# Kernel optimization log

Measured on AMD Instinct MI355X. Metric: run time of the kernel, lower is better.

Reference implementation:

```python
import jax, jax.numpy as jnp
import numpy as np
import math

NUM_LANDMARKS = 64
HEAD_DIM = 64
NUM_HEAD = 16
BATCH = 4
SEQ_LEN = 4096


def iterative_inv(mat, n_iter=6):
    # mat: [..., m, m]
    I = jnp.eye(mat.shape[-1], dtype=mat.dtype)
    K = mat
    # scalar normalization: global max of column sums * global max of row sums
    scale = 1.0 / (jnp.max(jnp.sum(jnp.abs(K), axis=-2)) * jnp.max(jnp.sum(jnp.abs(K), axis=-1)))
    V = scale * jnp.swapaxes(K, -1, -2)
    for _ in range(n_iter):
        KV = jnp.matmul(K, V)
        V = jnp.matmul(0.25 * V, 13.0 * I - jnp.matmul(KV, 15.0 * I - jnp.matmul(KV, 7.0 * I - KV)))
    return V


def setup_inputs() -> dict:
    key = jax.random.key(0)
    k1, k2, k3 = jax.random.split(key, 3)
    shape = (BATCH, NUM_HEAD, SEQ_LEN, HEAD_DIM)
    Q = jax.random.normal(k1, shape, dtype=jnp.float32)
    K = jax.random.normal(k2, shape, dtype=jnp.float32)
    V = jax.random.normal(k3, shape, dtype=jnp.float32)
    return {"Q": Q, "K": K, "V": V}


def reference(Q, K, V):
    seq_len = Q.shape[-2]
    m = NUM_LANDMARKS
    scale = 1.0 / math.sqrt(math.sqrt(HEAD_DIM))
    Q = Q * scale
    K = K * scale
    # landmark pooling: mean over contiguous segments of length seq_len // m
    seg = seq_len // m
    Q_lm = Q.reshape(-1, NUM_HEAD, m, seg, HEAD_DIM).mean(axis=-2)  # [B,H,m,d]
    K_lm = K.reshape(-1, NUM_HEAD, m, seg, HEAD_DIM).mean(axis=-2)  # [B,H,m,d]
    # three softmax kernels
    kernel_1 = jax.nn.softmax(jnp.einsum('bhsd,bhmd->bhsm', Q, K_lm), axis=-1)   # [B,H,S,m]
    kernel_2 = jax.nn.softmax(jnp.einsum('bhmd,bhnd->bhmn', Q_lm, K_lm), axis=-1)  # [B,H,m,m]
    kernel_3 = jax.nn.softmax(jnp.einsum('bhmd,bhsd->bhms', Q_lm, K), axis=-1)   # [B,H,m,S]
    inv_k2 = iterative_inv(kernel_2)
    X = jnp.matmul(jnp.matmul(kernel_1, inv_k2), jnp.matmul(kernel_3, V))  # [B,H,S,d]
    return X
```

## Files before the change

kernel.cpp:

```cpp
#include <hip/hip_runtime.h>
#include <hip/hip_bf16.h>

#define PAD 68
#define KP  72
#define SCALE 0.35355339059327379f

typedef __attribute__((ext_vector_type(8))) short bf16x8;
typedef __attribute__((ext_vector_type(4))) float f32x4;
#define MFMA_BF16 __builtin_amdgcn_mfma_f32_16x16x32_bf16

__device__ __forceinline__ short f2b(float f) {
    unsigned u = __float_as_uint(f);
    u += 0x7fff + ((u >> 16) & 1);
    return (short)(u >> 16);
}
__device__ __forceinline__ float b2f(short h) {
    return __uint_as_float(((unsigned)(unsigned short)h) << 16);
}

__device__ __forceinline__ void fma16(float acc[16], float a, const float* b) {
    const float4* b4 = reinterpret_cast<const float4*>(b);
    float4 x0 = b4[0], x1 = b4[1], x2 = b4[2], x3 = b4[3];
    acc[0]  += a * x0.x; acc[1]  += a * x0.y; acc[2]  += a * x0.z; acc[3]  += a * x0.w;
    acc[4]  += a * x1.x; acc[5]  += a * x1.y; acc[6]  += a * x1.z; acc[7]  += a * x1.w;
    acc[8]  += a * x2.x; acc[9]  += a * x2.y; acc[10] += a * x2.z; acc[11] += a * x2.w;
    acc[12] += a * x3.x; acc[13] += a * x3.y; acc[14] += a * x3.z; acc[15] += a * x3.w;
}

__device__ __forceinline__ void mm_tile(float acc[4][4],
                                        const float* __restrict__ A, int lda,
                                        const float* __restrict__ B,
                                        int i0, int j0) {
#pragma unroll
    for (int r = 0; r < 4; r++)
#pragma unroll
        for (int c = 0; c < 4; c++) acc[r][c] = 0.f;
#pragma unroll 4
    for (int k0 = 0; k0 < 64; k0 += 4) {
        float4 b0 = *reinterpret_cast<const float4*>(&B[(k0 + 0) * PAD + j0]);
        float4 b1 = *reinterpret_cast<const float4*>(&B[(k0 + 1) * PAD + j0]);
        float4 b2 = *reinterpret_cast<const float4*>(&B[(k0 + 2) * PAD + j0]);
        float4 b3 = *reinterpret_cast<const float4*>(&B[(k0 + 3) * PAD + j0]);
        float4 a0 = *reinterpret_cast<const float4*>(&A[(i0 + 0) * lda + k0]);
        float4 a1 = *reinterpret_cast<const float4*>(&A[(i0 + 1) * lda + k0]);
        float4 a2 = *reinterpret_cast<const float4*>(&A[(i0 + 2) * lda + k0]);
        float4 a3 = *reinterpret_cast<const float4*>(&A[(i0 + 3) * lda + k0]);
#define ROW_UPD(r, av) \
        acc[r][0] += av.x * b0.x + av.y * b1.x + av.z * b2.x + av.w * b3.x; \
        acc[r][1] += av.x * b0.y + av.y * b1.y + av.z * b2.y + av.w * b3.y; \
        acc[r][2] += av.x * b0.z + av.y * b1.z + av.z * b2.z + av.w * b3.z; \
        acc[r][3] += av.x * b0.w + av.y * b1.w + av.z * b2.w + av.w * b3.w;
        ROW_UPD(0, a0) ROW_UPD(1, a1) ROW_UPD(2, a2) ROW_UPD(3, a3)
#undef ROW_UPD
    }
}

__global__ __launch_bounds__(256) void pool_kernel(const float* __restrict__ Q,
                                                   const float* __restrict__ K,
                                                   float* __restrict__ Qlm,
                                                   float* __restrict__ Klm,
                                                   short* __restrict__ Qlm_b,
                                                   short* __restrict__ Klm_b) {
    __shared__ float4 red[256];
    const int blk = blockIdx.x;
    const int t = threadIdx.x;
    const int d4 = t & 15;
    const int rg = t >> 4;
    const float4* Q4 = reinterpret_cast<const float4*>(Q);
    const float4* K4 = reinterpret_cast<const float4*>(K);

    float4 sQ = {0.f, 0.f, 0.f, 0.f}, sK = {0.f, 0.f, 0.f, 0.f};
#pragma unroll
    for (int rr = 0; rr < 4; rr++) {
        int row = blk * 64 + rg * 4 + rr;
        int off4 = (row << 4) + d4;
        float4 q = Q4[off4], k = K4[off4];
        sQ.x += q.x; sQ.y += q.y; sQ.z += q.z; sQ.w += q.w;
        sK.x += k.x; sK.y += k.y; sK.z += k.z; sK.w += k.w;
    }
    const float c = SCALE * (1.0f / 64.0f);
    red[t] = sQ;
    __syncthreads();
    if (t < 16) {
        float4 s = {0.f, 0.f, 0.f, 0.f};
#pragma unroll
        for (int g = 0; g < 16; g++) {
            float4 v = red[g * 16 + t];
            s.x += v.x; s.y += v.y; s.z += v.z; s.w += v.w;
        }
        s.x *= c; s.y *= c; s.z *= c; s.w *= c;
        reinterpret_cast<float4*>(Qlm + blk * 64)[t] = s;
        ushort4 ub = { (unsigned short)f2b(s.x), (unsigned short)f2b(s.y),
                       (unsigned short)f2b(s.z), (unsigned short)f2b(s.w) };
        *reinterpret_cast<ushort4*>(&Qlm_b[blk * 64 + t * 4]) = ub;
    }
    __syncthreads();
    red[t] = sK;
    __syncthreads();
    if (t < 16) {
        float4 s = {0.f, 0.f, 0.f, 0.f};
#pragma unroll
        for (int g = 0; g < 16; g++) {
            float4 v = red[g * 16 + t];
            s.x += v.x; s.y += v.y; s.z += v.z; s.w += v.w;
        }
        s.x *= c; s.y *= c; s.z *= c; s.w *= c;
        reinterpret_cast<float4*>(Klm + blk * 64)[t] = s;
        ushort4 ub = { (unsigned short)f2b(s.x), (unsigned short)f2b(s.y),
                       (unsigned short)f2b(s.z), (unsigned short)f2b(s.w) };
        *reinterpret_cast<ushort4*>(&Klm_b[blk * 64 + t * 4]) = ub;
    }
}

__global__ __launch_bounds__(256) void k2_kernel(const float* __restrict__ Qlm,
                                                 const float* __restrict__ Klm,
                                                 float* __restrict__ K2g,
                                                 unsigned* __restrict__ colmax) {
    __shared__ float Ql[64 * PAD], Kl[64 * PAD], S2[64 * PAD];
    const int bh = blockIdx.x, t = threadIdx.x;
#pragma unroll
    for (int n = 0; n < 16; n++) {
        int f = t + n * 256;
        Ql[(f >> 6) * PAD + (f & 63)] = Qlm[bh * 4096 + f];
        Kl[(f >> 6) * PAD + (f & 63)] = Klm[bh * 4096 + f];
    }
    __syncthreads();
    const int i = t >> 2, j0 = (t & 3) * 16;
    float acc[16];
#pragma unroll
    for (int u = 0; u < 16; u++) acc[u] = 0.f;
    const float4* Ql4 = reinterpret_cast<const float4*>(Ql);
    const float4* Kl4 = reinterpret_cast<const float4*>(Kl);
    for (int k4 = 0; k4 < 16; k4++) {
        float4 a = Ql4[i * 17 + k4];
#pragma unroll
        for (int u = 0; u < 16; u++) {
            float4 b = Kl4[(j0 + u) * 17 + k4];
            acc[u] += a.x * b.x + a.y * b.y + a.z * b.z + a.w * b.w;
        }
    }
#pragma unroll
    for (int u = 0; u < 16; u++) S2[i * PAD + j0 + u] = acc[u];
    __syncthreads();
    if (t < 64) {
        float m = -1e30f;
        for (int j = 0; j < 64; j++) m = fmaxf(m, S2[t * PAD + j]);
        float sum = 0.f;
        for (int j = 0; j < 64; j++) {
            float e = __expf(S2[t * PAD + j] - m);
            S2[t * PAD + j] = e; sum += e;
        }
        float inv = 1.0f / sum;
        for (int j = 0; j < 64; j++) S2[t * PAD + j] *= inv;
    }
    __syncthreads();
#pragma unroll
    for (int n = 0; n < 16; n++) {
        int f = t + n * 256;
        K2g[bh * 4096 + f] = S2[(f >> 6) * PAD + (f & 63)];
    }
    if (t < 64) {
        float c = 0.f;
        for (int ii = 0; ii < 64; ii++) c += S2[ii * PAD + t];
        atomicMax(colmax, __float_as_uint(c));
    }
}

__global__ __launch_bounds__(256) void fused_inv_k3v(const short* __restrict__ Qlm_b,
                                                     const float* __restrict__ K,
                                                     const float* __restrict__ V,
                                                     float* __restrict__ W2acc,
                                                     float* __restrict__ rowsum3,
                                                     const float* __restrict__ K2g,
                                                     const unsigned* __restrict__ colmax,
                                                     float* __restrict__ K2invg) {
    __shared__ __align__(16) char smem[64 * PAD * 4 * 3];
    const int t = threadIdx.x;

    if (blockIdx.x < 64) {
        float* Vb = reinterpret_cast<float*>(smem);
        float* Ab = Vb + 64 * PAD;
        float* Tb = Ab + 64 * PAD;
        const int bh = blockIdx.x;
        const float sc = 1.0f / __uint_as_float(*colmax);
        const float* Kg = K2g + bh * 4096;
#pragma unroll
        for (int n = 0; n < 16; n++) {
            int f = t + n * 256;
            Vb[(f >> 6) * PAD + (f & 63)] = sc * Kg[(f & 63) * 64 + (f >> 6)];
        }
        __syncthreads();
        const int i0 = (t >> 4) * 4, j0 = (t & 15) * 4;
        float acc[4][4], vacc[4][4];
        for (int iter = 0; iter < 6; iter++) {
            mm_tile(acc, Kg, 64, Vb, i0, j0);
#pragma unroll
            for (int r = 0; r < 4; r++)
                *reinterpret_cast<float4*>(&Ab[(i0 + r) * PAD + j0]) =
                    make_float4(acc[r][0], acc[r][1], acc[r][2], acc[r][3]);
            __syncthreads();
            mm_tile(acc, Vb, PAD, Ab, i0, j0);
#pragma unroll
            for (int r = 0; r < 4; r++) {
                float4 v = *reinterpret_cast<const float4*>(&Vb[(i0 + r) * PAD + j0]);
                vacc[r][0] = 13.f * v.x - 15.f * acc[r][0];
                vacc[r][1] = 13.f * v.y - 15.f * acc[r][1];
                vacc[r][2] = 13.f * v.z - 15.f * acc[r][2];
                vacc[r][3] = 13.f * v.w - 15.f * acc[r][3];
                *reinterpret_cast<float4*>(&Tb[(i0 + r) * PAD + j0]) =
                    make_float4(acc[r][0], acc[r][1], acc[r][2], acc[r][3]);
            }
            __syncthreads();
            mm_tile(acc, Tb, PAD, Ab, i0, j0);
#pragma unroll
            for (int r = 0; r < 4; r++) {
                vacc[r][0] += 7.f * acc[r][0];
                vacc[r][1] += 7.f * acc[r][1];
                vacc[r][2] += 7.f * acc[r][2];
                vacc[r][3] += 7.f * acc[r][3];
                *reinterpret_cast<float4*>(&Vb[(i0 + r) * PAD + j0]) =
                    make_float4(acc[r][0], acc[r][1], acc[r][2], acc[r][3]);
            }
            __syncthreads();
            mm_tile(acc, Vb, PAD, Ab, i0, j0);
#pragma unroll
            for (int r = 0; r < 4; r++) {
                vacc[r][0] -= acc[r][0]; vacc[r][1] -= acc[r][1];
                vacc[r][2] -= acc[r][2]; vacc[r][3] -= acc[r][3];
            }
            __syncthreads();
#pragma unroll
            for (int r = 0; r < 4; r++)
                *reinterpret_cast<float4*>(&Vb[(i0 + r) * PAD + j0]) =
                    make_float4(0.25f * vacc[r][0], 0.25f * vacc[r][1],
                                0.25f * vacc[r][2], 0.25f * vacc[r][3]);
            __syncthreads();
        }
#pragma unroll
        for (int n = 0; n < 16; n++) {
            int f = t + n * 256;
            K2invg[bh * 4096 + f] = Vb[(f >> 6) * PAD + (f & 63)];
        }
        return;
    }

    short* Kt = reinterpret_cast<short*>(smem);
    short* Vt = Kt + 64 * KP;
    short* Eb = Vt + 64 * KP;
    const int idx = blockIdx.x - 64;
    const int chunk = idx & 31, bh = idx >> 5;
    const int w = t >> 6, lane = t & 63, quad = lane >> 4, l15 = lane & 15;
    const float4* K4 = reinterpret_cast<const float4*>(K);
    const float4* V4 = reinterpret_cast<const float4*>(V);
    const int dg = t & 15;
    const int kr = t >> 4;
    const int bhBase = bh * 4096;

    const bf16x8* Qb = reinterpret_cast<const bf16x8*>(Qlm_b + bh * 4096);
    bf16x8 a0 = Qb[(w * 16 + l15) * 8 + quad];
    bf16x8 a1 = Qb[(w * 16 + l15) * 8 + quad + 4];

    f32x4 oacc[4];
    float rsum[4];
#pragma unroll
    for (int nt = 0; nt < 4; nt++) { oacc[nt] = (f32x4){0.f, 0.f, 0.f, 0.f}; rsum[nt] = 0.f; }

    const int sb0 = chunk * 128;
    for (int tile = 0; tile < 2; tile++) {
        const int sb = sb0 + tile * 64;
        __syncthreads();
#pragma unroll
        for (int n = 0; n < 4; n++) {
            float4 kk = K4[(bhBase + sb + kr + 16 * n) * 16 + dg];
            ushort4 uk = { (unsigned short)f2b(SCALE * kk.x), (unsigned short)f2b(SCALE * kk.y),
                           (unsigned short)f2b(SCALE * kk.z), (unsigned short)f2b(SCALE * kk.w) };
            *reinterpret_cast<ushort4*>(&Kt[(kr + 16 * n) * KP + dg * 4]) = uk;
        }
        {
            float4 pv0 = V4[(bhBase + sb + kr * 4 + 0) * 16 + dg];
            float4 pv1 = V4[(bhBase + sb + kr * 4 + 1) * 16 + dg];
            float4 pv2 = V4[(bhBase + sb + kr * 4 + 2) * 16 + dg];
            float4 pv3 = V4[(bhBase + sb + kr * 4 + 3) * 16 + dg];
            ushort4 u0 = { (unsigned short)f2b(pv0.x), (unsigned short)f2b(pv1.x),
                           (unsigned short)f2b(pv2.x), (unsigned short)f2b(pv3.x) };
            ushort4 u1 = { (unsigned short)f2b(pv0.y), (unsigned short)f2b(pv1.y),
                           (unsigned short)f2b(pv2.y), (unsigned short)f2b(pv3.y) };
            ushort4 u2 = { (unsigned short)f2b(pv0.z), (unsigned short)f2b(pv1.z),
                           (unsigned short)f2b(pv2.z), (unsigned short)f2b(pv3.z) };
            ushort4 u3 = { (unsigned short)f2b(pv0.w), (unsigned short)f2b(pv1.w),
                           (unsigned short)f2b(pv2.w), (unsigned short)f2b(pv3.w) };
            *reinterpret_cast<ushort4*>(&Vt[(dg * 4 + 0) * KP + kr * 4]) = u0;
            *reinterpret_cast<ushort4*>(&Vt[(dg * 4 + 1) * KP + kr * 4]) = u1;
            *reinterpret_cast<ushort4*>(&Vt[(dg * 4 + 2) * KP + kr * 4]) = u2;
            *reinterpret_cast<ushort4*>(&Vt[(dg * 4 + 3) * KP + kr * 4]) = u3;
        }
        __syncthreads();
#pragma unroll
        for (int nt = 0; nt < 4; nt++) {
            bf16x8 b0 = *reinterpret_cast<const bf16x8*>(&Kt[(nt * 16 + l15) * KP + quad * 8]);
            bf16x8 b1 = *reinterpret_cast<const bf16x8*>(&Kt[(nt * 16 + l15) * KP + quad * 8 + 32]);
            f32x4 c = {0.f, 0.f, 0.f, 0.f};
            c = MFMA_BF16(a0, b0, c, 0, 0, 0);
            c = MFMA_BF16(a1, b1, c, 0, 0, 0);
#pragma unroll
            for (int reg = 0; reg < 4; reg++) {
                float e = __expf(c[reg]);
                rsum[reg] += e;
                Eb[(w * 16 + quad * 4 + reg) * KP + nt * 16 + l15] = f2b(e);
            }
        }
        bf16x8 e0 = *reinterpret_cast<const bf16x8*>(&Eb[(w * 16 + l15) * KP + quad * 8]);
        bf16x8 e1 = *reinterpret_cast<const bf16x8*>(&Eb[(w * 16 + l15) * KP + quad * 8 + 32]);
#pragma unroll
        for (int nt = 0; nt < 4; nt++) {
            bf16x8 b0 = *reinterpret_cast<const bf16x8*>(&Vt[(nt * 16 + l15) * KP + quad * 8]);
            bf16x8 b1 = *reinterpret_cast<const bf16x8*>(&Vt[(nt * 16 + l15) * KP + quad * 8 + 32]);
            oacc[nt] = MFMA_BF16(e0, b0, oacc[nt], 0, 0, 0);
            oacc[nt] = MFMA_BF16(e1, b1, oacc[nt], 0, 0, 0);
        }
    }
#pragma unroll
    for (int reg = 0; reg < 4; reg++) {
        float s = rsum[reg];
        s += __shfl_xor(s, 1); s += __shfl_xor(s, 2);
        s += __shfl_xor(s, 4); s += __shfl_xor(s, 8);
        rsum[reg] = s;
    }
    const int row0 = w * 16 + quad * 4;
    if (l15 == 0) {
#pragma unroll
        for (int reg = 0; reg < 4; reg++)
            atomicAdd(&rowsum3[bh * 64 + row0 + reg], rsum[reg]);
    }
#pragma unroll
    for (int nt = 0; nt < 4; nt++)
#pragma unroll
        for (int reg = 0; reg < 4; reg++)
            atomicAdd(&W2acc[(bh * 64 + row0 + reg) * 64 + nt * 16 + l15], oacc[nt][reg]);
}

__global__ __launch_bounds__(256) void wmid_kernel(const float* __restrict__ K2invg,
                                                   const float* __restrict__ W2acc,
                                                   const float* __restrict__ rowsum3,
                                                   short* __restrict__ Wth,
                                                   short* __restrict__ Wtl) {
    __shared__ float I1[64 * PAD], W2[64 * PAD];
    const int bh = blockIdx.x, t = threadIdx.x;
#pragma unroll
    for (int n = 0; n < 16; n++) {
        int f = t + n * 256;
        int r = f >> 6;
        I1[r * PAD + (f & 63)] = K2invg[bh * 4096 + f];
        W2[r * PAD + (f & 63)] = W2acc[bh * 4096 + f] / rowsum3[bh * 64 + r];
    }
    __syncthreads();
    const int i = t >> 2, j0 = (t & 3) * 16;
    float acc[16];
#pragma unroll
    for (int u = 0; u < 16; u++) acc[u] = 0.f;
    for (int k = 0; k < 64; k++) fma16(acc, I1[i * PAD + k], W2 + k * PAD + j0);
#pragma unroll
    for (int u = 0; u < 16; u++) {
        float wv = acc[u];
        short hi = f2b(wv);
        short lo = f2b(wv - b2f(hi));
        Wth[bh * 4096 + (j0 + u) * 64 + i] = hi;
        Wtl[bh * 4096 + (j0 + u) * 64 + i] = lo;
    }
}

__global__ __launch_bounds__(256) void final_mfma(const float* __restrict__ Q,
                                                  const short* __restrict__ Klm_b,
                                                  const short* __restrict__ Wth,
                                                  const short* __restrict__ Wtl,
                                                  float* __restrict__ out) {
    __shared__ short Eb[64 * KP];
    const int sc = blockIdx.x, bh = blockIdx.y, t = threadIdx.x;
    const int w = t >> 6, lane = t & 63, quad = lane >> 4, l15 = lane & 15;
    const int s0 = sc * 64;
    const int row = w * 16 + l15;

    const float* qrow = Q + ((size_t)bh * 4096 + s0 + row) * 64 + quad * 8;
    float4 qa = *reinterpret_cast<const float4*>(qrow);
    float4 qb = *reinterpret_cast<const float4*>(qrow + 4);
    float4 qc = *reinterpret_cast<const float4*>(qrow + 32);
    float4 qd = *reinterpret_cast<const float4*>(qrow + 36);

    const bf16x8* Kb = reinterpret_cast<const bf16x8*>(Klm_b + bh * 4096);
    const bf16x8* Hb = reinterpret_cast<const bf16x8*>(Wth + bh * 4096);
    const bf16x8* Lb = reinterpret_cast<const bf16x8*>(Wtl + bh * 4096);

    bf16x8 a0, a1;
    a0[0] = f2b(SCALE * qa.x); a0[1] = f2b(SCALE * qa.y);
    a0[2] = f2b(SCALE * qa.z); a0[3] = f2b(SCALE * qa.w);
    a0[4] = f2b(SCALE * qb.x); a0[5] = f2b(SCALE * qb.y);
    a0[6] = f2b(SCALE * qb.z); a0[7] = f2b(SCALE * qb.w);
    a1[0] = f2b(SCALE * qc.x); a1[1] = f2b(SCALE * qc.y);
    a1[2] = f2b(SCALE * qc.z); a1[3] = f2b(SCALE * qc.w);
    a1[4] = f2b(SCALE * qd.x); a1[5] = f2b(SCALE * qd.y);
    a1[6] = f2b(SCALE * qd.z); a1[7] = f2b(SCALE * qd.w);

    float rsum[4] = {0.f, 0.f, 0.f, 0.f};
#pragma unroll
    for (int nt = 0; nt < 4; nt++) {
        bf16x8 b0 = Kb[(nt * 16 + l15) * 8 + quad];
        bf16x8 b1 = Kb[(nt * 16 + l15) * 8 + quad + 4];
        f32x4 c = {0.f, 0.f, 0.f, 0.f};
        c = MFMA_BF16(a0, b0, c, 0, 0, 0);
        c = MFMA_BF16(a1, b1, c, 0, 0, 0);
#pragma unroll
        for (int reg = 0; reg < 4; reg++) {
            float e = __expf(c[reg]);
            rsum[reg] += e;
            Eb[(w * 16 + quad * 4 + reg) * KP + nt * 16 + l15] = f2b(e);
        }
    }
#pragma unroll
    for (int reg = 0; reg < 4; reg++) {
        float s = rsum[reg];
        s += __shfl_xor(s, 1); s += __shfl_xor(s, 2);
        s += __shfl_xor(s, 4); s += __shfl_xor(s, 8);
        rsum[reg] = 1.0f / s;
    }
    bf16x8 e0 = *reinterpret_cast<const bf16x8*>(&Eb[row * KP + quad * 8]);
    bf16x8 e1 = *reinterpret_cast<const bf16x8*>(&Eb[row * KP + quad * 8 + 32]);
    const int row0 = w * 16 + quad * 4;
#pragma unroll
    for (int nt = 0; nt < 4; nt++) {
        bf16x8 bh0 = Hb[(nt * 16 + l15) * 8 + quad];
        bf16x8 bh1 = Hb[(nt * 16 + l15) * 8 + quad + 4];
        bf16x8 bl0 = Lb[(nt * 16 + l15) * 8 + quad];
        bf16x8 bl1 = Lb[(nt * 16 + l15) * 8 + quad + 4];
        f32x4 c = {0.f, 0.f, 0.f, 0.f};
        c = MFMA_BF16(e0, bh0, c, 0, 0, 0);
        c = MFMA_BF16(e1, bh1, c, 0, 0, 0);
        c = MFMA_BF16(e0, bl0, c, 0, 0, 0);
        c = MFMA_BF16(e1, bl1, c, 0, 0, 0);
#pragma unroll
        for (int reg = 0; reg < 4; reg++)
            out[((size_t)bh * 4096 + s0 + row0 + reg) * 64 + nt * 16 + l15] = c[reg] * rsum[reg];
    }
}

extern "C" void kernel_launch(void* const* d_in, const int* in_sizes, int n_in,
                              void* d_out, int out_size, void* d_ws, size_t ws_size,
                              hipStream_t stream) {
    const float* Q = (const float*)d_in[0];
    const float* K = (const float*)d_in[1];
    const float* V = (const float*)d_in[2];
    float* out = (float*)d_out;
    float* ws = (float*)d_ws;

    float* Qlm     = ws;
    float* Klm     = ws + 262144;
    float* K2      = ws + 524288;
    float* K2inv   = ws + 786432;
    short* Wth     = (short*)(ws + 1048576);
    short* Wtl     = (short*)(ws + 1179648);
    float* W2acc   = ws + 1310720;
    float* rowsum3 = ws + 1572864;
    unsigned* colmax = (unsigned*)(ws + 1576960);
    short* Qlm_b   = (short*)(ws + 1576964);
    short* Klm_b   = (short*)(ws + 1708036);

    hipMemsetAsync(W2acc, 0, (262144 + 4096 + 1) * sizeof(float), stream);

    pool_kernel<<<4096, 256, 0, stream>>>(Q, K, Qlm, Klm, Qlm_b, Klm_b);
    k2_kernel<<<64, 256, 0, stream>>>(Qlm, Klm, K2, colmax);
    fused_inv_k3v<<<2112, 256, 0, stream>>>(Qlm_b, K, V, W2acc, rowsum3, K2, colmax, K2inv);
    wmid_kernel<<<64, 256, 0, stream>>>(K2inv, W2acc, rowsum3, Wth, Wtl);
    final_mfma<<<dim3(64, 64), 256, 0, stream>>>(Q, Klm_b, Wth, Wtl, out);
}
```

Baseline: 337.6 us.

## Run iterative inverse matmuls on bf16 MFMA with hi/lo split emulation

Replaces the FP32 scalar 64x64 matmuls in the Newton-Schulz inverse block with bf16 MFMA instructions. Each operand is split into high and low bf16 parts, and four cross products recover near-FP32 accuracy. Operands live in XOR-swizzled shared memory to avoid bank conflicts, and V stays in registers across iterations. The goal is to shorten the 64 inverse blocks, which may sit on the critical path alongside the k3v blocks. The cost is extra conversion work, a larger shared-memory footprint (64KB), and a possible accuracy loss from bf16x3-style emulation across 6 iterations.

```diff
diff --git a/kernel.cpp b/kernel.cpp
--- a/kernel.cpp
+++ b/kernel.cpp
@@ -27,32 +27,8 @@
     acc[12] += a * x3.x; acc[13] += a * x3.y; acc[14] += a * x3.z; acc[15] += a * x3.w;
 }
 
-__device__ __forceinline__ void mm_tile(float acc[4][4],
-                                        const float* __restrict__ A, int lda,
-                                        const float* __restrict__ B,
-                                        int i0, int j0) {
-#pragma unroll
-    for (int r = 0; r < 4; r++)
-#pragma unroll
-        for (int c = 0; c < 4; c++) acc[r][c] = 0.f;
-#pragma unroll 4
-    for (int k0 = 0; k0 < 64; k0 += 4) {
-        float4 b0 = *reinterpret_cast<const float4*>(&B[(k0 + 0) * PAD + j0]);
-        float4 b1 = *reinterpret_cast<const float4*>(&B[(k0 + 1) * PAD + j0]);
-        float4 b2 = *reinterpret_cast<const float4*>(&B[(k0 + 2) * PAD + j0]);
-        float4 b3 = *reinterpret_cast<const float4*>(&B[(k0 + 3) * PAD + j0]);
-        float4 a0 = *reinterpret_cast<const float4*>(&A[(i0 + 0) * lda + k0]);
-        float4 a1 = *reinterpret_cast<const float4*>(&A[(i0 + 1) * lda + k0]);
-        float4 a2 = *reinterpret_cast<const float4*>(&A[(i0 + 2) * lda + k0]);
-        float4 a3 = *reinterpret_cast<const float4*>(&A[(i0 + 3) * lda + k0]);
-#define ROW_UPD(r, av) \
-        acc[r][0] += av.x * b0.x + av.y * b1.x + av.z * b2.x + av.w * b3.x; \
-        acc[r][1] += av.x * b0.y + av.y * b1.y + av.z * b2.y + av.w * b3.y; \
-        acc[r][2] += av.x * b0.z + av.y * b1.z + av.z * b2.z + av.w * b3.z; \
-        acc[r][3] += av.x * b0.w + av.y * b1.w + av.z * b2.w + av.w * b3.w;
-        ROW_UPD(0, a0) ROW_UPD(1, a1) ROW_UPD(2, a2) ROW_UPD(3, a3)
-#undef ROW_UPD
-    }
+__device__ __forceinline__ int SWI(int row, int colS) {
+    return (((row << 7) + (colS << 1)) ^ ((row & 7) << 4)) >> 1;
 }
 
 __global__ __launch_bounds__(256) void pool_kernel(const float* __restrict__ Q,
@@ -174,73 +150,176 @@
                                                      const float* __restrict__ K2g,
                                                      const unsigned* __restrict__ colmax,
                                                      float* __restrict__ K2invg) {
-    __shared__ __align__(16) char smem[64 * PAD * 4 * 3];
+    __shared__ __align__(16) char smem[65536];
     const int t = threadIdx.x;
+    const int w = t >> 6, lane = t & 63, quad = lane >> 4, l15 = lane & 15;
 
     if (blockIdx.x < 64) {
-        float* Vb = reinterpret_cast<float*>(smem);
-        float* Ab = Vb + 64 * PAD;
-        float* Tb = Ab + 64 * PAD;
+        short* Krh = reinterpret_cast<short*>(smem);
+        short* Krl = Krh + 4096;
+        short* Ath = Krl + 4096;
+        short* Atl = Ath + 4096;
+        short* B1h = Atl + 4096;
+        short* B1l = B1h + 4096;
+        short* B2h = B1l + 4096;
+        short* B2l = B2h + 4096;
         const int bh = blockIdx.x;
-        const float sc = 1.0f / __uint_as_float(*colmax);
+        const float scv = 1.0f / __uint_as_float(*colmax);
         const float* Kg = K2g + bh * 4096;
-#pragma unroll
-        for (int n = 0; n < 16; n++) {
-            int f = t + n * 256;
-            Vb[(f >> 6) * PAD + (f & 63)] = sc * Kg[(f & 63) * 64 + (f >> 6)];
+
+#pragma unroll
+        for (int n = 0; n < 4; n++) {
+            int f4 = t + n * 256;
+            int r = f4 >> 4, c0 = (f4 & 15) * 4;
+            float4 kk = *reinterpret_cast<const float4*>(Kg + r * 64 + c0);
+            short h0 = f2b(kk.x), h1 = f2b(kk.y), h2 = f2b(kk.z), h3 = f2b(kk.w);
+            ushort4 uh = {(unsigned short)h0, (unsigned short)h1,
+                          (unsigned short)h2, (unsigned short)h3};
+            ushort4 ul = {(unsigned short)f2b(kk.x - b2f(h0)), (unsigned short)f2b(kk.y - b2f(h1)),
+                          (unsigned short)f2b(kk.z - b2f(h2)), (unsigned short)f2b(kk.w - b2f(h3))};
+            *reinterpret_cast<ushort4*>(&Krh[SWI(r, c0)]) = uh;
+            *reinterpret_cast<ushort4*>(&Krl[SWI(r, c0)]) = ul;
+            float s0 = scv * kk.x, s1 = scv * kk.y, s2 = scv * kk.z, s3 = scv * kk.w;
+            short g0 = f2b(s0), g1 = f2b(s1), g2 = f2b(s2), g3 = f2b(s3);
+            ushort4 vh = {(unsigned short)g0, (unsigned short)g1,
+                          (unsigned short)g2, (unsigned short)g3};
+            ushort4 vl = {(unsigned short)f2b(s0 - b2f(g0)), (unsigned short)f2b(s1 - b2f(g1)),
+                          (unsigned short)f2b(s2 - b2f(g2)), (unsigned short)f2b(s3 - b2f(g3))};
+            *reinterpret_cast<ushort4*>(&B1h[SWI(r, c0)]) = vh;
+            *reinterpret_cast<ushort4*>(&B1l[SWI(r, c0)]) = vl;
+            float t0 = scv * Kg[(c0 + 0) * 64 + r];
+            float t1 = scv * Kg[(c0 + 1) * 64 + r];
+            float t2 = scv * Kg[(c0 + 2) * 64 + r];
+            float t3 = scv * Kg[(c0 + 3) * 64 + r];
+            short e0 = f2b(t0), e1 = f2b(t1), e2 = f2b(t2), e3 = f2b(t3);
+            ushort4 th = {(unsigned short)e0, (unsigned short)e1,
+                          (unsigned short)e2, (unsigned short)e3};
+            ushort4 tl = {(unsigned short)f2b(t0 - b2f(e0)), (unsigned short)f2b(t1 - b2f(e1)),
+                          (unsigned short)f2b(t2 - b2f(e2)), (unsigned short)f2b(t3 - b2f(e3))};
+            *reinterpret_cast<ushort4*>(&B2h[SWI(r, c0)]) = th;
+            *reinterpret_cast<ushort4*>(&B2l[SWI(r, c0)]) = tl;
+        }
+        float vreg[4][4];
+#pragma unroll
+        for (int nt = 0; nt < 4; nt++) {
+            float4 vv = *reinterpret_cast<const float4*>(
+                Kg + (nt * 16 + l15) * 64 + w * 16 + quad * 4);
+            vreg[nt][0] = scv * vv.x; vreg[nt][1] = scv * vv.y;
+            vreg[nt][2] = scv * vv.z; vreg[nt][3] = scv * vv.w;
         }
         __syncthreads();
-        const int i0 = (t >> 4) * 4, j0 = (t & 15) * 4;
-        float acc[4][4], vacc[4][4];
+
+#define LOADA(Lh, Ll) \
+        bf16x8 ah0 = *reinterpret_cast<const bf16x8*>(&Lh[SWI(w * 16 + l15, quad * 8)]); \
+        bf16x8 ah1 = *reinterpret_cast<const bf16x8*>(&Lh[SWI(w * 16 + l15, quad * 8 + 32)]); \
+        bf16x8 al0 = *reinterpret_cast<const bf16x8*>(&Ll[SWI(w * 16 + l15, quad * 8)]); \
+        bf16x8 al1 = *reinterpret_cast<const bf16x8*>(&Ll[SWI(w * 16 + l15, quad * 8 + 32)]);
+#define PRODNT(Bh, Bl, nt, c) { \
+        bf16x8 bh0 = *reinterpret_cast<const bf16x8*>(&Bh[SWI(nt * 16 + l15, quad * 8)]); \
+        bf16x8 bh1 = *reinterpret_cast<const bf16x8*>(&Bh[SWI(nt * 16 + l15, quad * 8 + 32)]); \
+        bf16x8 bl0 = *reinterpret_cast<const bf16x8*>(&Bl[SWI(nt * 16 + l15, quad * 8)]); \
+        bf16x8 bl1 = *reinterpret_cast<const bf16x8*>(&Bl[SWI(nt * 16 + l15, quad * 8 + 32)]); \
+        c = MFMA_BF16(ah0, bh0, c, 0, 0, 0); c = MFMA_BF16(ah1, bh1, c, 0, 0, 0); \
+        c = MFMA_BF16(ah0, bl0, c, 0, 0, 0); c = MFMA_BF16(ah1, bl1, c, 0, 0, 0); \
+        c = MFMA_BF16(al0, bh0, c, 0, 0, 0); c = MFMA_BF16(al1, bh1, c, 0, 0, 0); \
+        c = MFMA_BF16(al0, bl0, c, 0, 0, 0); c = MFMA_BF16(al1, bl1, c, 0, 0, 0); }
+
         for (int iter = 0; iter < 6; iter++) {
-            mm_tile(acc, Kg, 64, Vb, i0, j0);
-#pragma unroll
-            for (int r = 0; r < 4; r++)
-                *reinterpret_cast<float4*>(&Ab[(i0 + r) * PAD + j0]) =
-                    make_float4(acc[r][0], acc[r][1], acc[r][2], acc[r][3]);
-            __syncthreads();
-            mm_tile(acc, Vb, PAD, Ab, i0, j0);
-#pragma unroll
-            for (int r = 0; r < 4; r++) {
-                float4 v = *reinterpret_cast<const float4*>(&Vb[(i0 + r) * PAD + j0]);
-                vacc[r][0] = 13.f * v.x - 15.f * acc[r][0];
-                vacc[r][1] = 13.f * v.y - 15.f * acc[r][1];
-                vacc[r][2] = 13.f * v.z - 15.f * acc[r][2];
-                vacc[r][3] = 13.f * v.w - 15.f * acc[r][3];
-                *reinterpret_cast<float4*>(&Tb[(i0 + r) * PAD + j0]) =
-                    make_float4(acc[r][0], acc[r][1], acc[r][2], acc[r][3]);
+            {
+                LOADA(Krh, Krl)
+#pragma unroll
+                for (int nt = 0; nt < 4; nt++) {
+                    f32x4 c = {0.f, 0.f, 0.f, 0.f};
+                    PRODNT(B1h, B1l, nt, c)
+                    short h0 = f2b(c[0]), h1 = f2b(c[1]), h2 = f2b(c[2]), h3 = f2b(c[3]);
+                    ushort4 uh = {(unsigned short)h0, (unsigned short)h1,
+                                  (unsigned short)h2, (unsigned short)h3};
+                    ushort4 ul = {(unsigned short)f2b(c[0] - b2f(h0)),
+                                  (unsigned short)f2b(c[1] - b2f(h1)),
+                                  (unsigned short)f2b(c[2] - b2f(h2)),
+                                  (unsigned short)f2b(c[3] - b2f(h3))};
+                    *reinterpret_cast<ushort4*>(&Ath[SWI(nt * 16 + l15, w * 16 + quad * 4)]) = uh;
+                    *reinterpret_cast<ushort4*>(&Atl[SWI(nt * 16 + l15, w * 16 + quad * 4)]) = ul;
+                }
             }
             __syncthreads();
-            mm_tile(acc, Tb, PAD, Ab, i0, j0);
-#pragma unroll
-            for (int r = 0; r < 4; r++) {
-                vacc[r][0] += 7.f * acc[r][0];
-                vacc[r][1] += 7.f * acc[r][1];
-                vacc[r][2] += 7.f * acc[r][2];
-                vacc[r][3] += 7.f * acc[r][3];
-                *reinterpret_cast<float4*>(&Vb[(i0 + r) * PAD + j0]) =
-                    make_float4(acc[r][0], acc[r][1], acc[r][2], acc[r][3]);
+            float p[4][4];
+            {
+                LOADA(B2h, B2l)
+#pragma unroll
+                for (int nt = 0; nt < 4; nt++) {
+                    f32x4 c = {0.f, 0.f, 0.f, 0.f};
+                    PRODNT(Ath, Atl, nt, c)
+#pragma unroll
+                    for (int reg = 0; reg < 4; reg++) {
+                        p[nt][reg] = c[reg];
+                        short hh = f2b(c[reg]);
+                        B1h[SWI(w * 16 + quad * 4 + reg, nt * 16 + l15)] = hh;
+                        B1l[SWI(w * 16 + quad * 4 + reg, nt * 16 + l15)] = f2b(c[reg] - b2f(hh));
+                    }
+                }
             }
             __syncthreads();
-            mm_tile(acc, Vb, PAD, Ab, i0, j0);
-#pragma unroll
-            for (int r = 0; r < 4; r++) {
-                vacc[r][0] -= acc[r][0]; vacc[r][1] -= acc[r][1];
-                vacc[r][2] -= acc[r][2]; vacc[r][3] -= acc[r][3];
+            float q[4][4];
+            {
+                LOADA(B1h, B1l)
+#pragma unroll
+                for (int nt = 0; nt < 4; nt++) {
+                    f32x4 c = {0.f, 0.f, 0.f, 0.f};
+                    PRODNT(Ath, Atl, nt, c)
+#pragma unroll
+                    for (int reg = 0; reg < 4; reg++) {
+                        q[nt][reg] = c[reg];
+                        short hh = f2b(c[reg]);
+                        B2h[SWI(w * 16 + quad * 4 + reg, nt * 16 + l15)] = hh;
+                        B2l[SWI(w * 16 + quad * 4 + reg, nt * 16 + l15)] = f2b(c[reg] - b2f(hh));
+                    }
+                }
             }
             __syncthreads();
-#pragma unroll
-            for (int r = 0; r < 4; r++)
-                *reinterpret_cast<float4*>(&Vb[(i0 + r) * PAD + j0]) =
-                    make_float4(0.25f * vacc[r][0], 0.25f * vacc[r][1],
-                                0.25f * vacc[r][2], 0.25f * vacc[r][3]);
+            {
+                LOADA(B2h, B2l)
+#pragma unroll
+                for (int nt = 0; nt < 4; nt++) {
+                    f32x4 c = {0.f, 0.f, 0.f, 0.f};
+                    PRODNT(Ath, Atl, nt, c)
+#pragma unroll
+                    for (int reg = 0; reg < 4; reg++)
+                        vreg[nt][reg] = 0.25f * (13.f * vreg[nt][reg] - 15.f * p[nt][reg]
+                                                 + 7.f * q[nt][reg] - c[reg]);
+                }
+            }
+#pragma unroll
+            for (int nt = 0; nt < 4; nt++) {
+                short h0 = f2b(vreg[nt][0]), h1 = f2b(vreg[nt][1]);
+                short h2 = f2b(vreg[nt][2]), h3 = f2b(vreg[nt][3]);
+                short g0 = f2b(vreg[nt][0] - b2f(h0)), g1 = f2b(vreg[nt][1] - b2f(h1));
+                short g2 = f2b(vreg[nt][2] - b2f(h2)), g3 = f2b(vreg[nt][3] - b2f(h3));
+                ushort4 uh = {(unsigned short)h0, (unsigned short)h1,
+                              (unsigned short)h2, (unsigned short)h3};
+                ushort4 ul = {(unsigned short)g0, (unsigned short)g1,
+                              (unsigned short)g2, (unsigned short)g3};
+                *reinterpret_cast<ushort4*>(&B1h[SWI(nt * 16 + l15, w * 16 + quad * 4)]) = uh;
+                *reinterpret_cast<ushort4*>(&B1l[SWI(nt * 16 + l15, w * 16 + quad * 4)]) = ul;
+                B2h[SWI(w * 16 + quad * 4 + 0, nt * 16 + l15)] = h0;
+                B2h[SWI(w * 16 + quad * 4 + 1, nt * 16 + l15)] = h1;
+                B2h[SWI(w * 16 + quad * 4 + 2, nt * 16 + l15)] = h2;
+                B2h[SWI(w * 16 + quad * 4 + 3, nt * 16 + l15)] = h3;
+                B2l[SWI(w * 16 + quad * 4 + 0, nt * 16 + l15)] = g0;
+                B2l[SWI(w * 16 + quad * 4 + 1, nt * 16 + l15)] = g1;
+                B2l[SWI(w * 16 + quad * 4 + 2, nt * 16 + l15)] = g2;
+                B2l[SWI(w * 16 + quad * 4 + 3, nt * 16 + l15)] = g3;
+            }
             __syncthreads();
         }
-#pragma unroll
-        for (int n = 0; n < 16; n++) {
-            int f = t + n * 256;
-            K2invg[bh * 4096 + f] = Vb[(f >> 6) * PAD + (f & 63)];
-        }
+#undef LOADA
+#undef PRODNT
+#pragma unroll
+        for (int nt = 0; nt < 4; nt++)
+#pragma unroll
+            for (int reg = 0; reg < 4; reg++)
+                K2invg[bh * 4096 + (w * 16 + quad * 4 + reg) * 64 + nt * 16 + l15] =
+                    vreg[nt][reg];
         return;
     }
 
@@ -249,7 +328,6 @@
     short* Eb = Vt + 64 * KP;
     const int idx = blockIdx.x - 64;
     const int chunk = idx & 31, bh = idx >> 5;
-    const int w = t >> 6, lane = t & 63, quad = lane >> 4, l15 = lane & 15;
     const float4* K4 = reinterpret_cast<const float4*>(K);
     const float4* V4 = reinterpret_cast<const float4*>(V);
     const int dg = t & 15;
```

Result: faster. 313.7 us (-7.1%).
